# Kernel tuning notes

Measured on AMD Instinct MI355X. Metric: run time of the kernel, lower is better.

The kernel has to match this reference:

```python
import jax, jax.numpy as jnp
import numpy as np

SEQ, B, E, H, V = 70, 128, 512, 1024, 10000


def setup_inputs() -> dict:
    key = jax.random.key(0)
    ks = jax.random.split(key, 24)
    u = lambda k, sh, a: jax.random.uniform(k, sh, jnp.float32, -a, a)
    kh = float(1.0 / np.sqrt(H))
    inp = {
        "inputs": jax.random.randint(ks[0], (SEQ, B), 0, V, dtype=jnp.int32),
        "hidden": jnp.zeros((2, B, H), jnp.float32),
        "emb_W": u(ks[1], (V, E), 0.1),
        "out_W": u(ks[2], (V, H), 0.1),
        "out_b": jnp.zeros((V,), jnp.float32),
    }
    i = 3
    for l, in_sz in enumerate([E, H]):
        for name, sh in [("Wir", (H, in_sz)), ("Wiz", (H, in_sz)), ("Wih", (H, in_sz)),
                         ("Whr", (H, H)), ("Whz", (H, H)), ("Whh", (H, H))]:
            inp[f"l{l}_{name}"] = u(ks[i], sh, kh); i += 1
        for name in ["bir", "biz", "bih"]:
            inp[f"l{l}_{name}"] = u(ks[i], (H,), kh); i += 1
    return inp


def gru_layer(xs, h0, Wir, bir, Whr, Wiz, biz, Whz, Wih, bih, Whh):
    # Precompute input-side projections for the whole sequence (big fused gemms).
    xr = jnp.einsum('sbe,he->sbh', xs, Wir) + bir  # (S,B,H)
    xz = jnp.einsum('sbe,he->sbh', xs, Wiz) + biz
    xh = jnp.einsum('sbe,he->sbh', xs, Wih) + bih

    def step(h, x_t):
        xr_t, xz_t, xh_t = x_t
        r = jax.nn.sigmoid(xr_t + h @ Whr.T)
        z = jax.nn.sigmoid(xz_t + h @ Whz.T)
        h1 = jnp.tanh(xh_t + r * (h @ Whh.T))
        h_new = (1.0 - z) * h1 + z * h
        return h_new, h_new

    hT, ys = jax.lax.scan(step, h0, (xr, xz, xh))
    return ys, hT


def reference(inputs, hidden, emb_W, out_W, out_b,
              l0_Wir, l0_Wiz, l0_Wih, l0_Whr, l0_Whz, l0_Whh, l0_bir, l0_biz, l0_bih,
              l1_Wir, l1_Wiz, l1_Wih, l1_Whr, l1_Whz, l1_Whh, l1_bir, l1_biz, l1_bih):
    emb = emb_W[inputs]  # (S,B,E)
    ys0, h0T = gru_layer(emb, hidden[0], l0_Wir, l0_bir, l0_Whr,
                         l0_Wiz, l0_biz, l0_Whz, l0_Wih, l0_bih, l0_Whh)
    ys1, h1T = gru_layer(ys0, hidden[1], l1_Wir, l1_bir, l1_Whr,
                         l1_Wiz, l1_biz, l1_Whz, l1_Wih, l1_bih, l1_Whh)
    logits = jnp.einsum('sbh,vh->sbv', ys1, out_W) + out_b  # (S,B,V)
    return logits, jnp.stack([h0T, h1T])
```

## Files before the change

kernel.cpp:

```cpp
#include <hip/hip_runtime.h>
#include <hip/hip_bf16.h>

#define SEQn 70
#define Bn 128
#define En 512
#define Hn 1024
#define Vn 10000
#define VPADn 10240
#define Mn (SEQn*Bn)
#define H3n (3*Hn)
#define BHn (Bn*Hn)
#define NBLK 192

typedef __hip_bfloat16 bf16;
typedef __attribute__((ext_vector_type(8))) short short8;
typedef __attribute__((ext_vector_type(4))) float f32x4;

__device__ __forceinline__ bf16 f2bf(float x){ return __float2bfloat16(x); }
__device__ __forceinline__ float bf2f(bf16 x){ return __bfloat162float(x); }

__device__ __forceinline__ void gl_lds16(const void* g, void* l){
  __builtin_amdgcn_global_load_lds((const __attribute__((address_space(1))) unsigned int*)g,
                                   (__attribute__((address_space(3))) unsigned int*)l, 16, 0, 0);
}


__global__ void cat3_w(const float* __restrict__ a, const float* __restrict__ b,
                       const float* __restrict__ c, bf16* __restrict__ d, int n){
  int i = blockIdx.x * 256 + threadIdx.x;
  if (i >= 3*n) return;
  const float* s = (i < n) ? a : ((i < 2*n) ? b : c);
  int off = (i < n) ? i : ((i < 2*n) ? i - n : i - 2*n);
  d[i] = f2bf(s[off]);
}

__global__ void cat3_f(const float* __restrict__ a, const float* __restrict__ b,
                       const float* __restrict__ c, float* __restrict__ d, int n){
  int i = blockIdx.x * 256 + threadIdx.x;
  if (i >= 3*n) return;
  d[i] = (i < n) ? a[i] : ((i < 2*n) ? b[i - n] : c[i - 2*n]);
}

__global__ void f2b_k(const float* __restrict__ s, bf16* __restrict__ d, int n){
  int i = blockIdx.x * 256 + threadIdx.x;
  if (i < n) d[i] = f2bf(s[i]);
}

__global__ void conv_outw(const float* __restrict__ s, bf16* __restrict__ d){
  long i = (long)blockIdx.x * 256 + threadIdx.x;
  if (i >= (long)VPADn * Hn) return;
  int row = (int)(i >> 10);
  d[i] = (row < Vn) ? f2bf(s[i]) : f2bf(0.f);
}

__global__ void embed_k(const int* __restrict__ idx, const float* __restrict__ eW,
                        bf16* __restrict__ out){
  const int sb = blockIdx.x;
  const int t = idx[sb];
  const float* s = eW + (long)t * En;
  bf16* d = out + (long)sb * En;
  for (int e = threadIdx.x; e < En; e += 256) d[e] = f2bf(s[e]);
}


template<bool OB, bool NB>
__global__ __launch_bounds__(256)
void gemm_bt(const bf16* __restrict__ A, const bf16* __restrict__ Bm,
             const float* __restrict__ bias, void* __restrict__ C,
             int K, int ldc, int nvalid)
{
  __shared__ __align__(16) bf16 As[128*64];
  __shared__ __align__(16) bf16 Bs[128*64];
  const int tid = threadIdx.x;
  const int l = tid & 63, w = tid >> 6;
  const int lr = l & 15, lk = l >> 4;
  const int wm = (w >> 1) * 64, wn = (w & 1) * 64;
  const int mt = blockIdx.y, nt = blockIdx.x;
  const bf16* Ag = A + (long)mt * 128 * K;
  const bf16* Bg = Bm + (long)nt * 128 * K;

  f32x4 acc[4][4] = {};

  for (int kb = 0; kb < K; kb += 64) {
#pragma unroll
    for (int r = 0; r < 4; ++r) {
      const int u = r * 256 + tid;
      const int row = u >> 3, kus = (u & 7) ^ (row & 7);
      gl_lds16(Ag + (long)row * K + kb + kus * 8, (char*)As + (r * 256 + w * 64) * 16);
    }
#pragma unroll
    for (int r = 0; r < 4; ++r) {
      const int u = r * 256 + tid;
      const int row = u >> 3, kus = (u & 7) ^ (row & 7);
      gl_lds16(Bg + (long)row * K + kb + kus * 8, (char*)Bs + (r * 256 + w * 64) * 16);
    }
    __syncthreads();
#pragma unroll
    for (int kh = 0; kh < 2; ++kh) {
      const int ku = kh * 4 + lk;
      short8 af[4], bfv[4];
#pragma unroll
      for (int i = 0; i < 4; ++i) {
        const int ar = wm + i * 16 + lr;
        af[i]  = *(const short8*)((const char*)As + ar * 128 + ((ku ^ (ar & 7)) * 16));
        const int br = wn + i * 16 + lr;
        bfv[i] = *(const short8*)((const char*)Bs + br * 128 + ((ku ^ (br & 7)) * 16));
      }
#pragma unroll
      for (int i = 0; i < 4; ++i)
#pragma unroll
        for (int j = 0; j < 4; ++j)
          acc[i][j] = __builtin_amdgcn_mfma_f32_16x16x32_bf16(af[i], bfv[j], acc[i][j], 0, 0, 0);
    }
    __syncthreads();
  }

#pragma unroll
  for (int i = 0; i < 4; ++i) {
#pragma unroll
    for (int j = 0; j < 4; ++j) {
      const int col = nt * 128 + wn + j * 16 + lr;
      const bool cok = (!NB) || (col < nvalid);
      const float bv = cok ? bias[col] : 0.f;
      const int row = mt * 128 + wm + i * 16 + lk * 4;
      if (cok) {
#pragma unroll
        for (int r = 0; r < 4; ++r) {
          const float v = acc[i][j][r] + bv;
          if (OB) ((bf16*)C)[(long)(row + r) * ldc + col] = f2bf(v);
          else    ((float*)C)[(long)(row + r) * ldc + col] = v;
        }
      }
    }
  }
}


#define LDGRP(bb, aa, cbase)                                                   \
  _Pragma("unroll")                                                            \
  for (int g = 0; g < 3; ++g)                                                  \
    _Pragma("unroll")                                                          \
    for (int j = 0; j < 4; ++j)                                                \
      bb[g][j] = *(const short8*)(smem +                                       \
          ((size_t)((g * 32 + (cbase) + j) * 64 + lane)) * 16);                \
  _Pragma("unroll")                                                            \
  for (int rt = 0; rt < 2; ++rt)                                               \
    _Pragma("unroll")                                                          \
    for (int j = 0; j < 4; ++j)                                                \
      aa[rt][j] = *(const short8*)(Arow[rt] + ((cbase) + j) * 32 + lk * 8);

#define MFGRP(bb, aa)                                                          \
  _Pragma("unroll")                                                            \
  for (int j = 0; j < 4; ++j)                                                  \
    _Pragma("unroll")                                                          \
    for (int rt = 0; rt < 2; ++rt)                                             \
      _Pragma("unroll")                                                        \
      for (int g = 0; g < 3; ++g)                                              \
        acc[rt][g] = __builtin_amdgcn_mfma_f32_16x16x32_bf16(                  \
            aa[rt][j], bb[g][j], acc[rt][g], 0, 0, 0);

__global__ __launch_bounds__(256, 1)
void gru_persist(const bf16* __restrict__ Wh0, const bf16* __restrict__ Wi1,
                 const bf16* __restrict__ Wh1, const float* __restrict__ b1,
                 const float* __restrict__ hidden, bf16* __restrict__ xg,
                 bf16* __restrict__ ys0, bf16* __restrict__ ys1,
                 float* __restrict__ hT, unsigned* __restrict__ bar)
{
  __shared__ __align__(16) char smem[98304];

  const int tid = threadIdx.x;
  const int lane = tid & 63, wid = tid >> 6;
  const int wbase = tid & ~63;
  const int lr = lane & 15, lk = lane >> 4;
  const int role = blockIdx.x >> 6, nb = blockIdx.x & 63;
  const int col0 = nb * 16;
  const int col = col0 + lr;

  unsigned myxcd;
  asm("s_getreg_b32 %0, hwreg(20, 0, 32)" : "=s"(myxcd));
  myxcd &= 7;
  unsigned* larrp  = bar + myxcd * 64;
  unsigned* gbarp  = bar + 512;
  unsigned* gflagp = bar + 544;

  const bf16* Wsrc = (role == 0) ? Wh0 : ((role == 1) ? Wi1 : Wh1);
#pragma unroll
  for (int it = 0; it < 24; ++it) {
    const int u0 = it * 256 + wbase;
    const int u  = u0 + lane;
    const int g  = u >> 11, c = (u >> 6) & 31, l = u & 63;
    gl_lds16(Wsrc + ((size_t)(g * Hn + col0 + (l & 15))) * Hn + c * 32 + (l >> 4) * 8,
             smem + (size_t)u0 * 16);
  }

  f32x4 hreg[2] = {};
  float bv[3] = {};
  if (role != 1) {
    const float* hsrc = hidden + (role == 2 ? BHn : 0);
#pragma unroll
    for (int rt = 0; rt < 2; ++rt)
#pragma unroll
      for (int r = 0; r < 4; ++r)
        hreg[rt][r] = hsrc[(size_t)((2 * wid + rt) * 16 + lk * 4 + r) * Hn + col];
  } else {
#pragma unroll
    for (int g = 0; g < 3; ++g) bv[g] = b1[g * Hn + col];
  }
  asm volatile("s_waitcnt vmcnt(0)" ::: "memory");
  __syncthreads();

  unsigned perxcd = 0;
  if (tid == 0) {
    (void)__hip_atomic_fetch_add(larrp, 1u, __ATOMIC_RELAXED, __HIP_MEMORY_SCOPE_WORKGROUP);
    asm volatile("s_waitcnt vmcnt(0)" ::: "memory");
    unsigned g = __hip_atomic_fetch_add(gbarp, 1u, __ATOMIC_RELAXED, __HIP_MEMORY_SCOPE_AGENT);
    if (g == NBLK - 1)
      __hip_atomic_store(gflagp, 1u, __ATOMIC_RELAXED, __HIP_MEMORY_SCOPE_AGENT);
    while (__hip_atomic_load(gflagp, __ATOMIC_RELAXED, __HIP_MEMORY_SCOPE_AGENT) < 1u)
      __builtin_amdgcn_s_sleep(2);
    perxcd = __hip_atomic_fetch_add(larrp, 0u, __ATOMIC_RELAXED, __HIP_MEMORY_SCOPE_WORKGROUP);
  }
  __syncthreads();

  for (int s = 0; s < 72; ++s) {
    const int t = s - role;
    if (t >= 0 && t < SEQn) {
      const bf16* Asrc = (role == 0) ? (ys0 + (size_t)t * BHn)
                       : (role == 1) ? (ys0 + (size_t)(t + 1) * BHn)
                                     : (ys1 + (size_t)t * BHn);
      const bf16* Arow[2];
      Arow[0] = Asrc + (size_t)((2 * wid) * 16 + lr) * Hn;
      Arow[1] = Asrc + (size_t)((2 * wid + 1) * 16 + lr) * Hn;
      f32x4 acc[2][3] = {};
      short8 bA[3][4], bB[3][4], aA[2][4], aB[2][4];
      unsigned short xus[2][12];

      LDGRP(bA, aA, 0)
      LDGRP(bB, aB, 4)
      if (role != 1) {
        const bf16* xsrc = xg + (size_t)t * Bn * (size_t)H3n;
#pragma unroll
        for (int rt = 0; rt < 2; ++rt)
#pragma unroll
          for (int g = 0; g < 3; ++g)
#pragma unroll
            for (int r = 0; r < 4; ++r) {
              const int row = (2 * wid + rt) * 16 + lk * 4 + r;
              const unsigned short* p =
                  (const unsigned short*)(xsrc + (size_t)row * H3n + g * Hn + col);
              xus[rt][g * 4 + r] = (role == 2)
                ? __hip_atomic_load((unsigned short*)p, __ATOMIC_RELAXED, __HIP_MEMORY_SCOPE_AGENT)
                : *p;
            }
      }
      MFGRP(bA, aA) LDGRP(bA, aA, 8)
      MFGRP(bB, aB) LDGRP(bB, aB, 12)
      MFGRP(bA, aA) LDGRP(bA, aA, 16)
      MFGRP(bB, aB) LDGRP(bB, aB, 20)
      MFGRP(bA, aA) LDGRP(bA, aA, 24)
      MFGRP(bB, aB) LDGRP(bB, aB, 28)
      MFGRP(bA, aA)
      MFGRP(bB, aB)

      if (role == 1) {
#pragma unroll
        for (int rt = 0; rt < 2; ++rt)
#pragma unroll
          for (int g = 0; g < 3; ++g)
#pragma unroll
            for (int r = 0; r < 4; ++r) {
              const int row = (2 * wid + rt) * 16 + lk * 4 + r;
              unsigned short v = __builtin_bit_cast(unsigned short, f2bf(acc[rt][g][r] + bv[g]));
              __hip_atomic_store(
                  (unsigned short*)&xg[((size_t)t * Bn + row) * H3n + g * Hn + col],
                  v, __ATOMIC_RELAXED, __HIP_MEMORY_SCOPE_AGENT);
            }
      } else {
        bf16* ydst = ((role == 0) ? ys0 : ys1) + (size_t)(t + 1) * BHn;
#pragma unroll
        for (int rt = 0; rt < 2; ++rt)
#pragma unroll
          for (int r = 0; r < 4; ++r) {
            const int row = (2 * wid + rt) * 16 + lk * 4 + r;
            const float xr = bf2f(__builtin_bit_cast(bf16, xus[rt][r]));
            const float xz = bf2f(__builtin_bit_cast(bf16, xus[rt][4 + r]));
            const float xh = bf2f(__builtin_bit_cast(bf16, xus[rt][8 + r]));
            const float rg = 1.f / (1.f + __expf(-(xr + acc[rt][0][r])));
            const float zg = 1.f / (1.f + __expf(-(xz + acc[rt][1][r])));
            const float hc = tanhf(xh + rg * acc[rt][2][r]);
            const float hn = (1.f - zg) * hc + zg * hreg[rt][r];
            hreg[rt][r] = hn;
            unsigned short v = __builtin_bit_cast(unsigned short, f2bf(hn));
            __hip_atomic_store((unsigned short*)&ydst[(size_t)row * Hn + col],
                               v, __ATOMIC_RELAXED, __HIP_MEMORY_SCOPE_AGENT);
            if (t == SEQn - 1)
              hT[(role == 0 ? 0 : BHn) + (size_t)row * Hn + col] = hn;
          }
      }
    }
    if (s < 71) {
      __syncthreads();
      if (tid == 0) {
        unsigned a = __hip_atomic_fetch_add(larrp, 1u, __ATOMIC_RELAXED,
                                            __HIP_MEMORY_SCOPE_WORKGROUP);
        if (a == perxcd * (unsigned)(s + 2) - 1u) {
          unsigned g = __hip_atomic_fetch_add(gbarp, perxcd, __ATOMIC_RELAXED,
                                              __HIP_MEMORY_SCOPE_AGENT);
          if (g + perxcd == (unsigned)NBLK * (unsigned)(s + 2))
            __hip_atomic_store(gflagp, (unsigned)(s + 2), __ATOMIC_RELAXED,
                               __HIP_MEMORY_SCOPE_AGENT);
        }
        while (__hip_atomic_load(gflagp, __ATOMIC_RELAXED,
                                 __HIP_MEMORY_SCOPE_AGENT) < (unsigned)(s + 2))
          __builtin_amdgcn_s_sleep(2);
      }
      __syncthreads();
    }
  }
}


extern "C" void kernel_launch(void* const* d_in, const int* in_sizes, int n_in,
                              void* d_out, int out_size, void* d_ws, size_t ws_size,
                              hipStream_t stream)
{
  (void)in_sizes; (void)n_in; (void)out_size; (void)ws_size;
  const int*   inp    = (const int*)d_in[0];
  const float* hidden = (const float*)d_in[1];
  const float* embW   = (const float*)d_in[2];
  const float* outW   = (const float*)d_in[3];
  const float* outb   = (const float*)d_in[4];

  char* p = (char*)d_ws;
  auto take = [&](size_t n){ char* q = p; p += (n + 255) & ~(size_t)255; return q; };
  bf16*  l0Wi = (bf16*) take((size_t)H3n*En*2);
  bf16*  l0Wh = (bf16*) take((size_t)H3n*Hn*2);
  bf16*  l1Wi = (bf16*) take((size_t)H3n*Hn*2);
  bf16*  l1Wh = (bf16*) take((size_t)H3n*Hn*2);
  bf16*  oW   = (bf16*) take((size_t)VPADn*Hn*2);
  float* b0   = (float*)take((size_t)H3n*4);
  float* b1   = (float*)take((size_t)H3n*4);
  bf16*  emb  = (bf16*) take((size_t)Mn*En*2);
  bf16*  xg   = (bf16*) take((size_t)Mn*H3n*2);
  bf16*  ys0  = (bf16*) take((size_t)(SEQn+1)*BHn*2);
  bf16*  ys1  = (bf16*) take((size_t)(SEQn+1)*BHn*2);
  unsigned* bar = (unsigned*)take(4096);

  cat3_w<<<dim3((3*Hn*En+255)/256),256,0,stream>>>((const float*)d_in[5],(const float*)d_in[6],(const float*)d_in[7], l0Wi, Hn*En);
  cat3_w<<<dim3((3*Hn*Hn+255)/256),256,0,stream>>>((const float*)d_in[8],(const float*)d_in[9],(const float*)d_in[10], l0Wh, Hn*Hn);
  cat3_w<<<dim3((3*Hn*Hn+255)/256),256,0,stream>>>((const float*)d_in[14],(const float*)d_in[15],(const float*)d_in[16], l1Wi, Hn*Hn);
  cat3_w<<<dim3((3*Hn*Hn+255)/256),256,0,stream>>>((const float*)d_in[17],(const float*)d_in[18],(const float*)d_in[19], l1Wh, Hn*Hn);
  conv_outw<<<dim3((unsigned)(((long)VPADn*Hn+255)/256)),256,0,stream>>>(outW, oW);
  cat3_f<<<dim3((H3n+255)/256),256,0,stream>>>((const float*)d_in[11],(const float*)d_in[12],(const float*)d_in[13], b0, Hn);
  cat3_f<<<dim3((H3n+255)/256),256,0,stream>>>((const float*)d_in[20],(const float*)d_in[21],(const float*)d_in[22], b1, Hn);
  f2b_k<<<dim3((BHn+255)/256),256,0,stream>>>(hidden, ys0, BHn);
  f2b_k<<<dim3((BHn+255)/256),256,0,stream>>>(hidden + BHn, ys1, BHn);
  embed_k<<<dim3(Mn),256,0,stream>>>(inp, embW, emb);
  hipMemsetAsync(bar, 0, 4096, stream);

  gemm_bt<true,false><<<dim3(H3n/128, Mn/128),256,0,stream>>>(emb, l0Wi, b0, xg, En, H3n, H3n);

  float* hT = (float*)d_out + (size_t)SEQn * Bn * Vn;
  gru_persist<<<dim3(NBLK), 256, 0, stream>>>(l0Wh, l1Wi, l1Wh, b1, hidden,
                                              xg, ys0, ys1, hT, bar);

  gemm_bt<false,true><<<dim3(VPADn/128, Mn/128),256,0,stream>>>(ys1 + BHn, oW, outb, d_out, Hn, Vn, Vn);
}
```

Baseline: 1.133 ms.

## Replace global lockstep grid barrier with per-role dataflow flags in persistent GRU

All 192 blocks used to meet at one grid-wide barrier every step, with the three roles (layer-0 recurrence, layer-1 input projection, layer-1 recurrence) skewed by one step each. Now each role keeps its own per-XCD and global counters and a completion flag. Each role waits only on the flags it depends on: its own previous step, and the upstream role's step t+1. Roles can run ahead of one another, the loop runs 70 steps instead of 72, and the contention of a single 192-way barrier goes away. The cost is that correctness now rests on the relaxed-atomic flag ordering and the xg reuse between role0 reads and role1 writes.

```diff
diff --git a/kernel.cpp b/kernel.cpp
--- a/kernel.cpp
+++ b/kernel.cpp
@@ -179,9 +179,12 @@
   unsigned myxcd;
   asm("s_getreg_b32 %0, hwreg(20, 0, 32)" : "=s"(myxcd));
   myxcd &= 7;
-  unsigned* larrp  = bar + myxcd * 64;
-  unsigned* gbarp  = bar + 512;
-  unsigned* gflagp = bar + 544;
+  unsigned* Lp = bar + (role * 8 + (int)myxcd) * 32;
+  unsigned* Gi = bar + 768;
+  unsigned* Fi = bar + 800;
+  unsigned* Gr = bar + 832 + role * 32;
+  unsigned* Fr = bar + 928 + role * 32;
+  unsigned* Fdep = bar + 928 + (role - 1) * 32;
 
   const bf16* Wsrc = (role == 0) ? Wh0 : ((role == 1) ? Wi1 : Wh1);
 #pragma unroll
@@ -211,110 +214,119 @@
 
   unsigned perxcd = 0;
   if (tid == 0) {
-    (void)__hip_atomic_fetch_add(larrp, 1u, __ATOMIC_RELAXED, __HIP_MEMORY_SCOPE_WORKGROUP);
+    (void)__hip_atomic_fetch_add(Lp, 1u, __ATOMIC_RELAXED, __HIP_MEMORY_SCOPE_WORKGROUP);
     asm volatile("s_waitcnt vmcnt(0)" ::: "memory");
-    unsigned g = __hip_atomic_fetch_add(gbarp, 1u, __ATOMIC_RELAXED, __HIP_MEMORY_SCOPE_AGENT);
+    unsigned g = __hip_atomic_fetch_add(Gi, 1u, __ATOMIC_RELAXED, __HIP_MEMORY_SCOPE_AGENT);
     if (g == NBLK - 1)
-      __hip_atomic_store(gflagp, 1u, __ATOMIC_RELAXED, __HIP_MEMORY_SCOPE_AGENT);
-    while (__hip_atomic_load(gflagp, __ATOMIC_RELAXED, __HIP_MEMORY_SCOPE_AGENT) < 1u)
+      __hip_atomic_store(Fi, 1u, __ATOMIC_RELAXED, __HIP_MEMORY_SCOPE_AGENT);
+    while (__hip_atomic_load(Fi, __ATOMIC_RELAXED, __HIP_MEMORY_SCOPE_AGENT) < 1u)
       __builtin_amdgcn_s_sleep(2);
-    perxcd = __hip_atomic_fetch_add(larrp, 0u, __ATOMIC_RELAXED, __HIP_MEMORY_SCOPE_WORKGROUP);
+    perxcd = __hip_atomic_fetch_add(Lp, 0u, __ATOMIC_RELAXED, __HIP_MEMORY_SCOPE_WORKGROUP);
   }
   __syncthreads();
 
-  for (int s = 0; s < 72; ++s) {
-    const int t = s - role;
-    if (t >= 0 && t < SEQn) {
-      const bf16* Asrc = (role == 0) ? (ys0 + (size_t)t * BHn)
-                       : (role == 1) ? (ys0 + (size_t)(t + 1) * BHn)
-                                     : (ys1 + (size_t)t * BHn);
-      const bf16* Arow[2];
-      Arow[0] = Asrc + (size_t)((2 * wid) * 16 + lr) * Hn;
-      Arow[1] = Asrc + (size_t)((2 * wid + 1) * 16 + lr) * Hn;
-      f32x4 acc[2][3] = {};
-      short8 bA[3][4], bB[3][4], aA[2][4], aB[2][4];
-      unsigned short xus[2][12];
-
-      LDGRP(bA, aA, 0)
-      LDGRP(bB, aB, 4)
-      if (role != 1) {
-        const bf16* xsrc = xg + (size_t)t * Bn * (size_t)H3n;
-#pragma unroll
-        for (int rt = 0; rt < 2; ++rt)
-#pragma unroll
-          for (int g = 0; g < 3; ++g)
-#pragma unroll
-            for (int r = 0; r < 4; ++r) {
-              const int row = (2 * wid + rt) * 16 + lk * 4 + r;
-              const unsigned short* p =
-                  (const unsigned short*)(xsrc + (size_t)row * H3n + g * Hn + col);
-              xus[rt][g * 4 + r] = (role == 2)
-                ? __hip_atomic_load((unsigned short*)p, __ATOMIC_RELAXED, __HIP_MEMORY_SCOPE_AGENT)
-                : *p;
-            }
+  for (int t = 0; t < SEQn; ++t) {
+    if (tid == 0) {
+      if (role == 0) {
+        while (__hip_atomic_load(Fr, __ATOMIC_RELAXED, __HIP_MEMORY_SCOPE_AGENT) < (unsigned)t)
+          __builtin_amdgcn_s_sleep(1);
+      } else if (role == 1) {
+        while (__hip_atomic_load(Fdep, __ATOMIC_RELAXED, __HIP_MEMORY_SCOPE_AGENT) < (unsigned)(t + 1))
+          __builtin_amdgcn_s_sleep(1);
+      } else {
+        while (__hip_atomic_load(Fdep, __ATOMIC_RELAXED, __HIP_MEMORY_SCOPE_AGENT) < (unsigned)(t + 1))
+          __builtin_amdgcn_s_sleep(1);
+        while (__hip_atomic_load(Fr, __ATOMIC_RELAXED, __HIP_MEMORY_SCOPE_AGENT) < (unsigned)t)
+          __builtin_amdgcn_s_sleep(1);
       }
-      MFGRP(bA, aA) LDGRP(bA, aA, 8)
-      MFGRP(bB, aB) LDGRP(bB, aB, 12)
-      MFGRP(bA, aA) LDGRP(bA, aA, 16)
-      MFGRP(bB, aB) LDGRP(bB, aB, 20)
-      MFGRP(bA, aA) LDGRP(bA, aA, 24)
-      MFGRP(bB, aB) LDGRP(bB, aB, 28)
-      MFGRP(bA, aA)
-      MFGRP(bB, aB)
-
-      if (role == 1) {
-#pragma unroll
-        for (int rt = 0; rt < 2; ++rt)
-#pragma unroll
-          for (int g = 0; g < 3; ++g)
-#pragma unroll
-            for (int r = 0; r < 4; ++r) {
-              const int row = (2 * wid + rt) * 16 + lk * 4 + r;
-              unsigned short v = __builtin_bit_cast(unsigned short, f2bf(acc[rt][g][r] + bv[g]));
-              __hip_atomic_store(
-                  (unsigned short*)&xg[((size_t)t * Bn + row) * H3n + g * Hn + col],
-                  v, __ATOMIC_RELAXED, __HIP_MEMORY_SCOPE_AGENT);
-            }
-      } else {
-        bf16* ydst = ((role == 0) ? ys0 : ys1) + (size_t)(t + 1) * BHn;
-#pragma unroll
-        for (int rt = 0; rt < 2; ++rt)
+    }
+    __syncthreads();
+
+    const bf16* Asrc = (role == 0) ? (ys0 + (size_t)t * BHn)
+                     : (role == 1) ? (ys0 + (size_t)(t + 1) * BHn)
+                                   : (ys1 + (size_t)t * BHn);
+    const bf16* Arow[2];
+    Arow[0] = Asrc + (size_t)((2 * wid) * 16 + lr) * Hn;
+    Arow[1] = Asrc + (size_t)((2 * wid + 1) * 16 + lr) * Hn;
+    f32x4 acc[2][3] = {};
+    short8 bA[3][4], bB[3][4], aA[2][4], aB[2][4];
+    unsigned short xus[2][12];
+
+    LDGRP(bA, aA, 0)
+    LDGRP(bB, aB, 4)
+    if (role != 1) {
+      const bf16* xsrc = xg + (size_t)t * Bn * (size_t)H3n;
+#pragma unroll
+      for (int rt = 0; rt < 2; ++rt)
+#pragma unroll
+        for (int g = 0; g < 3; ++g)
 #pragma unroll
           for (int r = 0; r < 4; ++r) {
             const int row = (2 * wid + rt) * 16 + lk * 4 + r;
-            const float xr = bf2f(__builtin_bit_cast(bf16, xus[rt][r]));
-            const float xz = bf2f(__builtin_bit_cast(bf16, xus[rt][4 + r]));
-            const float xh = bf2f(__builtin_bit_cast(bf16, xus[rt][8 + r]));
-            const float rg = 1.f / (1.f + __expf(-(xr + acc[rt][0][r])));
-            const float zg = 1.f / (1.f + __expf(-(xz + acc[rt][1][r])));
-            const float hc = tanhf(xh + rg * acc[rt][2][r]);
-            const float hn = (1.f - zg) * hc + zg * hreg[rt][r];
-            hreg[rt][r] = hn;
-            unsigned short v = __builtin_bit_cast(unsigned short, f2bf(hn));
-            __hip_atomic_store((unsigned short*)&ydst[(size_t)row * Hn + col],
-                               v, __ATOMIC_RELAXED, __HIP_MEMORY_SCOPE_AGENT);
-            if (t == SEQn - 1)
-              hT[(role == 0 ? 0 : BHn) + (size_t)row * Hn + col] = hn;
+            const unsigned short* p =
+                (const unsigned short*)(xsrc + (size_t)row * H3n + g * Hn + col);
+            xus[rt][g * 4 + r] = (role == 2)
+              ? __hip_atomic_load((unsigned short*)p, __ATOMIC_RELAXED, __HIP_MEMORY_SCOPE_AGENT)
+              : *p;
           }
+    }
+    MFGRP(bA, aA) LDGRP(bA, aA, 8)
+    MFGRP(bB, aB) LDGRP(bB, aB, 12)
+    MFGRP(bA, aA) LDGRP(bA, aA, 16)
+    MFGRP(bB, aB) LDGRP(bB, aB, 20)
+    MFGRP(bA, aA) LDGRP(bA, aA, 24)
+    MFGRP(bB, aB) LDGRP(bB, aB, 28)
+    MFGRP(bA, aA)
+    MFGRP(bB, aB)
+
+    if (role == 1) {
+#pragma unroll
+      for (int rt = 0; rt < 2; ++rt)
+#pragma unroll
+        for (int g = 0; g < 3; ++g)
+#pragma unroll
+          for (int r = 0; r < 4; ++r) {
+            const int row = (2 * wid + rt) * 16 + lk * 4 + r;
+            unsigned short v = __builtin_bit_cast(unsigned short,
+                                                  f2bf(acc[rt][g][r] + bv[g]));
+            __hip_atomic_store(
+                (unsigned short*)&xg[((size_t)t * Bn + row) * H3n + g * Hn + col],
+                v, __ATOMIC_RELAXED, __HIP_MEMORY_SCOPE_AGENT);
+          }
+    } else {
+      bf16* ydst = ((role == 0) ? ys0 : ys1) + (size_t)(t + 1) * BHn;
+#pragma unroll
+      for (int rt = 0; rt < 2; ++rt)
+#pragma unroll
+        for (int r = 0; r < 4; ++r) {
+          const int row = (2 * wid + rt) * 16 + lk * 4 + r;
+          const float xr = bf2f(__builtin_bit_cast(bf16, xus[rt][r]));
+          const float xz = bf2f(__builtin_bit_cast(bf16, xus[rt][4 + r]));
+          const float xh = bf2f(__builtin_bit_cast(bf16, xus[rt][8 + r]));
+          const float rg = 1.f / (1.f + __expf(-(xr + acc[rt][0][r])));
+          const float zg = 1.f / (1.f + __expf(-(xz + acc[rt][1][r])));
+          const float hc = tanhf(xh + rg * acc[rt][2][r]);
+          const float hn = (1.f - zg) * hc + zg * hreg[rt][r];
+          hreg[rt][r] = hn;
+          unsigned short v = __builtin_bit_cast(unsigned short, f2bf(hn));
+          __hip_atomic_store((unsigned short*)&ydst[(size_t)row * Hn + col],
+                             v, __ATOMIC_RELAXED, __HIP_MEMORY_SCOPE_AGENT);
+          if (t == SEQn - 1)
+            hT[(role == 0 ? 0 : BHn) + (size_t)row * Hn + col] = hn;
+        }
+    }
+
+    __syncthreads();
+    if (tid == 0) {
+      unsigned a = __hip_atomic_fetch_add(Lp, 1u, __ATOMIC_RELAXED,
+                                          __HIP_MEMORY_SCOPE_WORKGROUP);
+      if (a == perxcd * (unsigned)(t + 2) - 1u) {
+        unsigned g = __hip_atomic_fetch_add(Gr, perxcd, __ATOMIC_RELAXED,
+                                            __HIP_MEMORY_SCOPE_AGENT);
+        if (g + perxcd == 64u * (unsigned)(t + 1))
+          __hip_atomic_store(Fr, (unsigned)(t + 1), __ATOMIC_RELAXED,
+                             __HIP_MEMORY_SCOPE_AGENT);
       }
-    }
-    if (s < 71) {
-      __syncthreads();
-      if (tid == 0) {
-        unsigned a = __hip_atomic_fetch_add(larrp, 1u, __ATOMIC_RELAXED,
-                                            __HIP_MEMORY_SCOPE_WORKGROUP);
-        if (a == perxcd * (unsigned)(s + 2) - 1u) {
-          unsigned g = __hip_atomic_fetch_add(gbarp, perxcd, __ATOMIC_RELAXED,
-                                              __HIP_MEMORY_SCOPE_AGENT);
-          if (g + perxcd == (unsigned)NBLK * (unsigned)(s + 2))
-            __hip_atomic_store(gflagp, (unsigned)(s + 2), __ATOMIC_RELAXED,
-                               __HIP_MEMORY_SCOPE_AGENT);
-        }
-        while (__hip_atomic_load(gflagp, __ATOMIC_RELAXED,
-                                 __HIP_MEMORY_SCOPE_AGENT) < (unsigned)(s + 2))
-          __builtin_amdgcn_s_sleep(2);
-      }
-      __syncthreads();
     }
   }
 }
@@ -356,7 +368,7 @@
   f2b_k<<<dim3((BHn+255)/256),256,0,stream>>>(hidden, ys0, BHn);
   f2b_k<<<dim3((BHn+255)/256),256,0,stream>>>(hidden + BHn, ys1, BHn);
   embed_k<<<dim3(Mn),256,0,stream>>>(inp, embW, emb);
-  hipMemsetAsync(bar, 0, 4096, stream);
+  (void)hipMemsetAsync(bar, 0, 4096, stream);
 
   gemm_bt<true,false><<<dim3(H3n/128, Mn/128),256,0,stream>>>(emb, l0Wi, b0, xg, En, H3n, H3n);
 
```

Result: no change. 1.127 ms (-0.6%).
